# Kernel optimization log

Hardware: AMD Instinct MI355X
Metric: run time of the kernel (lower is better)

## Reference

```python
import jax, jax.numpy as jnp
import numpy as np

N = 100000      # nodes
E = 3200000     # edges (avg degree 32)
IN = 256        # in_channels
HID = 32        # hidden (hard-coded in module)
OUT = 40        # out_channels / classes
BN_EPS = 1e-5


def gcn_conv(x, W, b, src, dst, n):
    # PyG GCNConv: h = x @ W; add self-loops; symmetric norm D^-1/2 A D^-1/2; aggregate; + bias
    h = x @ W                                   # [n, d_out]
    loop = jnp.arange(n)
    s = jnp.concatenate([src, loop])            # [E+n]
    d = jnp.concatenate([dst, loop])
    deg = jax.ops.segment_sum(jnp.ones_like(d, dtype=h.dtype), d, num_segments=n)
    dinv = jnp.where(deg > 0, jax.lax.rsqrt(deg), 0.0)
    norm = dinv[s] * dinv[d]                    # [E+n]
    msg = h[s] * norm[:, None]                  # gather + scale
    return jax.ops.segment_sum(msg, d, num_segments=n) + b


def setup_inputs() -> dict:
    key = jax.random.key(0)
    k = jax.random.split(key, 4)
    x = jax.random.normal(k[0], (N, IN), dtype=jnp.float32)
    edge_index = jax.random.randint(k[1], (2, E), 0, N, dtype=jnp.int64)
    W1 = jax.random.normal(k[2], (IN, HID), dtype=jnp.float32) / np.float32(np.sqrt(IN))
    b1 = jnp.zeros((HID,), jnp.float32)
    W2 = jax.random.normal(k[3], (HID, OUT), dtype=jnp.float32) / np.float32(np.sqrt(HID))
    b2 = jnp.zeros((OUT,), jnp.float32)
    return {"x": x, "edge_index": edge_index, "W1": W1, "b1": b1, "W2": W2, "b2": b2}


def reference(x, edge_index, W1, b1, W2, b2):
    src, dst = edge_index[0], edge_index[1]
    h = jax.nn.elu(gcn_conv(x, W1, b1, src, dst, N))
    # BatchNorm1d created fresh each forward: batch stats, gamma=1, beta=0 (biased var)
    mean = jnp.mean(h, axis=0)
    var = jnp.mean((h - mean) ** 2, axis=0)
    h = (h - mean) * jax.lax.rsqrt(var + BN_EPS)
    h = jax.nn.relu(h)
    # Dropout(p=0.2): identity in eval / deterministic reference
    out = gcn_conv(h, W2, b2, src, dst, N)
    return jax.nn.log_softmax(out, axis=-1)
```

## Files before the change

kernel.cpp:

```cpp
#include <hip/hip_runtime.h>
#include <math.h>

typedef unsigned int uint;
typedef unsigned short ushort;
typedef float v2f __attribute__((ext_vector_type(2)));

__device__ __forceinline__ v2f fp8lo_to_f32(uint u) {
    return __builtin_amdgcn_cvt_pk_f32_fp8((int)u, false);
}
__device__ __forceinline__ v2f fp8hi_to_f32(uint u) {
    return __builtin_amdgcn_cvt_pk_f32_fp8((int)u, true);
}
__device__ __forceinline__ ushort f32x2_to_fp8(float a, float b) {
    return (ushort)(__builtin_amdgcn_cvt_pk_fp8_f32(a, b, 0, false) & 0xffff);
}

#define UNPACK8(r, f)                                                  \
    {                                                                  \
        v2f p0_ = fp8lo_to_f32((r).x), p1_ = fp8hi_to_f32((r).x);      \
        v2f p2_ = fp8lo_to_f32((r).y), p3_ = fp8hi_to_f32((r).y);      \
        f[0] += p0_.x; f[1] += p0_.y; f[2] += p1_.x; f[3] += p1_.y;    \
        f[4] += p2_.x; f[5] += p2_.y; f[6] += p3_.x; f[7] += p3_.y;    \
    }

#define NBU 49
#define NSEG 4
#define CELL 17408
#define SUBCAP 1280
#define CSRCAP 4608

__global__ __launch_bounds__(256) void k_bin(
    const int* __restrict__ src, const int* __restrict__ dst,
    int* __restrict__ cur, uint* __restrict__ ebuf, int E) {
    __shared__ int hist[NBU], base_[NBU], off[NBU];
    int tid = threadIdx.x;
    if (tid < NBU) { hist[tid] = 0; off[tid] = 0; }
    __syncthreads();
    int e0 = blockIdx.x * 4096 + tid;
    int s_[16], d_[16];
#pragma unroll
    for (int j = 0; j < 16; ++j) {
        int e = e0 + j * 256;
        if (e < E) {
            s_[j] = src[e]; d_[j] = dst[e];
            atomicAdd(&hist[d_[j] >> 11], 1);
        } else d_[j] = -1;
    }
    __syncthreads();
    int seg = blockIdx.x & 3;
    if (tid < NBU && hist[tid])
        base_[tid] = atomicAdd(&cur[tid * NSEG + seg], hist[tid]);
    __syncthreads();
#pragma unroll
    for (int j = 0; j < 16; ++j) {
        if (d_[j] >= 0) {
            int b = d_[j] >> 11;
            int p = base_[b] + atomicAdd(&off[b], 1);
            if (p < CELL)
                ebuf[(size_t)(b * NSEG + seg) * CELL + p] =
                    ((uint)(d_[j] & 2047) << 17) | (uint)s_[j];
        }
    }
}

__global__ __launch_bounds__(256) void k_bin2(
    const int* __restrict__ cur, const uint* __restrict__ ebuf,
    uint* __restrict__ subcell, int* __restrict__ slotlen) {
    __shared__ int curs[16], sbase[16];
    int tid = threadIdx.x;
    int b = blockIdx.x >> 2, seg = blockIdx.x & 3;
    if (tid < 16) {
        int sb = ((b * 16 + tid) * NSEG + seg) * SUBCAP;
        sbase[tid] = sb;
        curs[tid] = sb;
    }
    __syncthreads();
    int len = cur[b * NSEG + seg]; if (len > CELL) len = CELL;
    const uint* ep = ebuf + (size_t)(b * NSEG + seg) * CELL;
    int i = tid;
    for (; i + 768 < len; i += 1024) {
        uint v0 = ep[i], v1 = ep[i + 256], v2 = ep[i + 512], v3 = ep[i + 768];
        int u0 = (v0 >> 24) & 15, u1 = (v1 >> 24) & 15;
        int u2 = (v2 >> 24) & 15, u3 = (v3 >> 24) & 15;
        int p0 = atomicAdd(&curs[u0], 1);
        if (p0 - sbase[u0] < SUBCAP) subcell[p0] = v0;
        int p1 = atomicAdd(&curs[u1], 1);
        if (p1 - sbase[u1] < SUBCAP) subcell[p1] = v1;
        int p2 = atomicAdd(&curs[u2], 1);
        if (p2 - sbase[u2] < SUBCAP) subcell[p2] = v2;
        int p3 = atomicAdd(&curs[u3], 1);
        if (p3 - sbase[u3] < SUBCAP) subcell[p3] = v3;
    }
    for (; i < len; i += 256) {
        uint v = ep[i];
        int u = (v >> 24) & 15;
        int p = atomicAdd(&curs[u], 1);
        if (p - sbase[u] < SUBCAP) subcell[p] = v;
    }
    __syncthreads();
    if (tid < 16) {
        int c = curs[tid] - sbase[tid];
        slotlen[(b * 16 + tid) * NSEG + seg] = c < SUBCAP ? c : SUBCAP;
    }
}

__global__ __launch_bounds__(256) void k_sort3(
    const int* __restrict__ slotlen, const uint* __restrict__ subcell,
    uint* __restrict__ csr, int* __restrict__ rowstart, int* __restrict__ deg,
    float* __restrict__ dinv, int n) {
    __shared__ int hist[128];
    __shared__ int wtot;
    int tid = threadIdx.x;
    int bs = blockIdx.x;
    if (tid < 128) hist[tid] = 0;
    __syncthreads();
    int lens[NSEG];
    const uint* sp = subcell + (size_t)bs * NSEG * SUBCAP;
    for (int s = 0; s < NSEG; ++s) {
        int len = slotlen[bs * NSEG + s];
        lens[s] = len;
        const uint* ep = sp + s * SUBCAP;
        int i = tid;
        for (; i + 768 < len; i += 1024) {
            uint v0 = ep[i], v1 = ep[i + 256], v2 = ep[i + 512], v3 = ep[i + 768];
            atomicAdd(&hist[(v0 >> 17) & 127], 1);
            atomicAdd(&hist[(v1 >> 17) & 127], 1);
            atomicAdd(&hist[(v2 >> 17) & 127], 1);
            atomicAdd(&hist[(v3 >> 17) & 127], 1);
        }
        for (; i < len; i += 256) atomicAdd(&hist[(ep[i] >> 17) & 127], 1);
    }
    __syncthreads();
    int c = (tid < 128) ? hist[tid] : 0;
    int lane = tid & 63, w = tid >> 6;
    int incl = c;
#pragma unroll
    for (int o = 1; o < 64; o <<= 1) {
        int t = __shfl_up(incl, o, 64);
        if (lane >= o) incl += t;
    }
    if (w == 0 && lane == 63) wtot = incl;
    __syncthreads();
    int excl = incl - c + ((w == 1) ? wtot : 0);
    int csrBase = bs * CSRCAP;
    int node = bs * 128 + tid;
    if (tid < 128 && node < n) {
        deg[node] = c;
        dinv[node] = rsqrtf((float)c + 1.0f);
        rowstart[node] = csrBase + excl;
    }
    __syncthreads();
    if (tid < 128) hist[tid] = excl;
    __syncthreads();
    for (int s = 0; s < NSEG; ++s) {
        const uint* ep = sp + s * SUBCAP;
        int len = lens[s];
        int i = tid;
        for (; i + 768 < len; i += 1024) {
            uint v0 = ep[i], v1 = ep[i + 256], v2 = ep[i + 512], v3 = ep[i + 768];
            int p0 = atomicAdd(&hist[(v0 >> 17) & 127], 1);
            csr[csrBase + p0] = v0 & 0x1FFFFu;
            int p1 = atomicAdd(&hist[(v1 >> 17) & 127], 1);
            csr[csrBase + p1] = v1 & 0x1FFFFu;
            int p2 = atomicAdd(&hist[(v2 >> 17) & 127], 1);
            csr[csrBase + p2] = v2 & 0x1FFFFu;
            int p3 = atomicAdd(&hist[(v3 >> 17) & 127], 1);
            csr[csrBase + p3] = v3 & 0x1FFFFu;
        }
        for (; i < len; i += 256) {
            uint v = ep[i];
            int p = atomicAdd(&hist[(v >> 17) & 127], 1);
            csr[csrBase + p] = v & 0x1FFFFu;
        }
    }
}


__global__ __launch_bounds__(256) void k_gemm1(
    const float* __restrict__ x, const float* __restrict__ W,
    const float* __restrict__ dinv, ushort* __restrict__ h8, int n) {
    __shared__ ushort xl[64 * 256];
    int tid = threadIdx.x;
    int node0 = blockIdx.x * 64;

#pragma unroll 4
    for (int i = 0; i < 16; ++i) {
        int fidx = i * 1024 + tid * 4;
        int row = fidx >> 8, k = fidx & 255;
        uint bx = 0, by = 0;
        if (node0 + row < n) {
            float4 xv = *(const float4*)(x + (size_t)(node0 + row) * 256 + k);
            uint r0 = (__float_as_uint(xv.x) + 0x8000u) >> 16;
            uint r1 = (__float_as_uint(xv.y) + 0x8000u) >> 16;
            uint r2 = (__float_as_uint(xv.z) + 0x8000u) >> 16;
            uint r3 = (__float_as_uint(xv.w) + 0x8000u) >> 16;
            bx = r0 | (r1 << 16); by = r2 | (r3 << 16);
        }
        int g = k >> 3;
        int byteoff = row * 512 + (((g ^ (row & 31)) << 4) | ((k & 7) << 1));
        *(uint2*)((char*)xl + byteoff) = make_uint2(bx, by);
    }
    __syncthreads();

    int lane = tid & 63;
    int wv = __builtin_amdgcn_readfirstlane(tid >> 6);
    const char* xrow = (const char*)xl + lane * 512;
    int rx = lane & 31;
    const float* Wp = W + wv * 8;
    float acc[8];
#pragma unroll
    for (int c = 0; c < 8; ++c) acc[c] = 0.f;
#pragma unroll 2
    for (int g = 0; g < 32; ++g) {
        uint4 q = *(const uint4*)(xrow + (((g ^ rx) << 4)));
        float xe[8];
        xe[0] = __uint_as_float(q.x << 16);
        xe[1] = __uint_as_float(q.x & 0xFFFF0000u);
        xe[2] = __uint_as_float(q.y << 16);
        xe[3] = __uint_as_float(q.y & 0xFFFF0000u);
        xe[4] = __uint_as_float(q.z << 16);
        xe[5] = __uint_as_float(q.z & 0xFFFF0000u);
        xe[6] = __uint_as_float(q.w << 16);
        xe[7] = __uint_as_float(q.w & 0xFFFF0000u);
        const float* w0 = Wp + (size_t)(g * 8) * 32;
#pragma unroll
        for (int e = 0; e < 8; ++e) {
#pragma unroll
            for (int c = 0; c < 8; ++c) acc[c] += xe[e] * w0[e * 32 + c];
        }
    }
    int node = node0 + lane;
    if (node < n) {
        float di = dinv[node];
        ushort u0 = f32x2_to_fp8(acc[0] * di, acc[1] * di);
        ushort u1 = f32x2_to_fp8(acc[2] * di, acc[3] * di);
        ushort u2 = f32x2_to_fp8(acc[4] * di, acc[5] * di);
        ushort u3 = f32x2_to_fp8(acc[6] * di, acc[7] * di);
        uint2 p;
        p.x = (uint)u0 | ((uint)u1 << 16);
        p.y = (uint)u2 | ((uint)u3 << 16);
        *((uint2*)(h8 + (size_t)node * 16) + wv) = p;
    }
}

__global__ __launch_bounds__(256) void k_agg1(
    const ushort* __restrict__ hs, const int* __restrict__ deg,
    const int* __restrict__ rowstart, const uint* __restrict__ csr,
    const float* __restrict__ dinv, const float* __restrict__ b1,
    ushort* __restrict__ y, float* __restrict__ partials, int n) {
    int tid = threadIdx.x;
    int l4 = tid & 3;
    int g  = tid >> 2;
    int d  = blockIdx.x * 64 + g;
    float sa[8], qa[8];
#pragma unroll
    for (int j = 0; j < 8; ++j) { sa[j] = 0.f; qa[j] = 0.f; }
    if (d < n) {
        float a[8], c[8];
#pragma unroll
        for (int j = 0; j < 8; ++j) { a[j] = 0.f; c[j] = 0.f; }
        uint2 sr = *((const uint2*)(hs + (size_t)d * 16) + l4);
        UNPACK8(sr, a);
        const uint* row = csr + rowstart[d];
        int end = deg[d];
        int k = 0;
        for (; k + 4 <= end; k += 4) {
            uint s0 = row[k], s1 = row[k+1], s2 = row[k+2], s3 = row[k+3];
            uint2 r0 = *((const uint2*)(hs + (size_t)s0 * 16) + l4);
            uint2 r1 = *((const uint2*)(hs + (size_t)s1 * 16) + l4);
            uint2 r2 = *((const uint2*)(hs + (size_t)s2 * 16) + l4);
            uint2 r3 = *((const uint2*)(hs + (size_t)s3 * 16) + l4);
            UNPACK8(r0, a); UNPACK8(r1, c);
            UNPACK8(r2, a); UNPACK8(r3, c);
        }
        for (; k < end; ++k) {
            uint2 r = *((const uint2*)(hs + (size_t)row[k] * 16) + l4);
            UNPACK8(r, a);
        }
        float di = dinv[d];
        float4 bA = *(const float4*)(b1 + l4 * 8);
        float4 bB = *(const float4*)(b1 + l4 * 8 + 4);
        float bv[8] = {bA.x, bA.y, bA.z, bA.w, bB.x, bB.y, bB.z, bB.w};
        float vv[8];
#pragma unroll
        for (int j = 0; j < 8; ++j) {
            float v = di * (a[j] + c[j]) + bv[j];
            v = v > 0.f ? v : expm1f(v);
            vv[j] = v; sa[j] = v; qa[j] = v * v;
        }
        ushort u0 = f32x2_to_fp8(vv[0], vv[1]);
        ushort u1 = f32x2_to_fp8(vv[2], vv[3]);
        ushort u2 = f32x2_to_fp8(vv[4], vv[5]);
        ushort u3 = f32x2_to_fp8(vv[6], vv[7]);
        uint2 pw;
        pw.x = (uint)u0 | ((uint)u1 << 16);
        pw.y = (uint)u2 | ((uint)u3 << 16);
        *((uint2*)(y + (size_t)d * 16) + l4) = pw;
    }
#pragma unroll
    for (int m = 4; m <= 32; m <<= 1) {
#pragma unroll
        for (int j = 0; j < 8; ++j) {
            sa[j] += __shfl_xor(sa[j], m, 64);
            qa[j] += __shfl_xor(qa[j], m, 64);
        }
    }
    __shared__ float wred[4][4][16];
    int lane = tid & 63, wv = tid >> 6;
    if (lane < 4) {
#pragma unroll
        for (int j = 0; j < 8; ++j) {
            wred[wv][lane][j]     = sa[j];
            wred[wv][lane][8 + j] = qa[j];
        }
    }
    __syncthreads();
    if (tid < 64) {
        int l4g = tid >> 4, slot = tid & 15;
        partials[(size_t)blockIdx.x * 64 + tid] =
            wred[0][l4g][slot] + wred[1][l4g][slot] +
            wred[2][l4g][slot] + wred[3][l4g][slot];
    }
}

__global__ __launch_bounds__(1024) void k_red(
    const float* __restrict__ partials, float* __restrict__ stats, int nblk) {
    __shared__ float red[1024];
    int t = threadIdx.x;
    int j = t & 63, w = t >> 6;
    float a = 0.f;
    for (int i = w; i < nblk; i += 16) a += partials[(size_t)i * 64 + j];
    red[t] = a;
    __syncthreads();
    if (t < 64) {
        float v = 0.f;
#pragma unroll
        for (int kk = 0; kk < 16; ++kk) v += red[kk * 64 + t];
        int l4g = t >> 4, slot = t & 15, c = l4g * 8 + (slot & 7);
        stats[(slot < 8) ? c : (32 + c)] = v;
    }
}

__global__ void k_bn2(const ushort* __restrict__ y, const float* __restrict__ stats,
                      const float* __restrict__ dinv, ushort* __restrict__ h2s, int n) {
    int t = blockIdx.x * blockDim.x + threadIdx.x;
    if (t >= n * 16) return;
    int i = t >> 4, c2 = (t & 15) * 2;
    float invn = 1.0f / (float)n;
    float m0 = stats[c2] * invn,    m1 = stats[c2+1] * invn;
    float v0 = stats[32+c2] * invn - m0*m0;
    float v1 = stats[33+c2] * invn - m1*m1;
    float s0 = rsqrtf(v0 + 1e-5f), s1 = rsqrtf(v1 + 1e-5f);
    float di = dinv[i];
    v2f u = fp8lo_to_f32(y[t]);
    float a = (u.x - m0) * s0; a = a > 0.f ? a : 0.f; a *= di;
    float b = (u.y - m1) * s1; b = b > 0.f ? b : 0.f; b *= di;
    h2s[t] = f32x2_to_fp8(a, b);
}

__global__ __launch_bounds__(256) void k_agg2(
    const ushort* __restrict__ h2s, const int* __restrict__ deg,
    const int* __restrict__ rowstart, const uint* __restrict__ csr,
    const float* __restrict__ dinv, const float* __restrict__ W2,
    const float* __restrict__ b2, float* __restrict__ out, int n) {
    __shared__ float w2s[1280];
    __shared__ float b2s[40];
    __shared__ float tb[64][33];
    int tid = threadIdx.x;
    for (int t = tid; t < 1280; t += 256) w2s[t] = W2[t];
    if (tid < 40) b2s[tid] = b2[tid];
    int l4 = tid & 3, g = tid >> 2;
    int d = blockIdx.x * 64 + g;
    if (d < n) {
        float a[8], c[8];
#pragma unroll
        for (int j = 0; j < 8; ++j) { a[j] = 0.f; c[j] = 0.f; }
        uint2 sr = *((const uint2*)(h2s + (size_t)d * 16) + l4);
        UNPACK8(sr, a);
        const uint* row = csr + rowstart[d];
        int end = deg[d];
        int k = 0;
        for (; k + 4 <= end; k += 4) {
            uint s0 = row[k], s1 = row[k+1], s2 = row[k+2], s3 = row[k+3];
            uint2 r0 = *((const uint2*)(h2s + (size_t)s0 * 16) + l4);
            uint2 r1 = *((const uint2*)(h2s + (size_t)s1 * 16) + l4);
            uint2 r2 = *((const uint2*)(h2s + (size_t)s2 * 16) + l4);
            uint2 r3 = *((const uint2*)(h2s + (size_t)s3 * 16) + l4);
            UNPACK8(r0, a); UNPACK8(r1, c);
            UNPACK8(r2, a); UNPACK8(r3, c);
        }
        for (; k < end; ++k) {
            uint2 r = *((const uint2*)(h2s + (size_t)row[k] * 16) + l4);
            UNPACK8(r, a);
        }
        float di = dinv[d];
#pragma unroll
        for (int j = 0; j < 8; ++j) tb[g][l4 * 8 + j] = di * (a[j] + c[j]);
    }
    __syncthreads();
    float o[10];
    const float* bp = b2s + l4 * 10;
#pragma unroll
    for (int m = 0; m < 10; ++m) o[m] = bp[m];
#pragma unroll
    for (int cc = 0; cc < 32; ++cc) {
        float tc = tb[g][cc];
        const float* wr = w2s + cc * 40 + l4 * 10;
#pragma unroll
        for (int m = 0; m < 10; ++m) o[m] += tc * wr[m];
    }
    float mx = o[0];
#pragma unroll
    for (int m = 1; m < 10; ++m) mx = fmaxf(mx, o[m]);
    mx = fmaxf(mx, __shfl_xor(mx, 1, 64));
    mx = fmaxf(mx, __shfl_xor(mx, 2, 64));
    float s = 0.f;
#pragma unroll
    for (int m = 0; m < 10; ++m) s += __expf(o[m] - mx);
    s += __shfl_xor(s, 1, 64);
    s += __shfl_xor(s, 2, 64);
    float lse = mx + __logf(s);
    if (d < n) {
        float* r = out + (size_t)d * 40 + l4 * 10;
#pragma unroll
        for (int m = 0; m < 10; m += 2) {
            float2 wv;
            wv.x = o[m] - lse; wv.y = o[m+1] - lse;
            *(float2*)(r + m) = wv;
        }
    }
}


extern "C" void kernel_launch(void* const* d_in, const int* in_sizes, int n_in,
                              void* d_out, int out_size, void* d_ws, size_t ws_size,
                              hipStream_t stream) {
    const float* x  = (const float*)d_in[0];
    const int*   ei = (const int*)d_in[1];
    const float* W1 = (const float*)d_in[2];
    const float* b1 = (const float*)d_in[3];
    const float* W2 = (const float*)d_in[4];
    const float* b2 = (const float*)d_in[5];

    int n = in_sizes[0] / 256;
    int E = in_sizes[1] / 2;
    const int* src = ei;
    const int* dst = ei + E;

    char*   base    = (char*)d_ws;
    ushort* hs8     = (ushort*)base;
    ushort* y       = (ushort*)(base + (size_t)n * 32);
    ushort* h2s     = (ushort*)(base + (size_t)n * 64);
    float*  dinv    = (float*) (base + (size_t)n * 96);
    int*    deg     = (int*)   (base + (size_t)n * 100);
    int*    rowstart= (int*)   (base + (size_t)n * 104);
    float*  stats   = (float*) (base + (size_t)n * 108);
    int*    cur     = (int*)   (base + (size_t)n * 108 + 256);
    int*    slotlen = (int*)   (base + (size_t)n * 108 + 1280);
    float*  partials= (float*) (base + (size_t)n * 108 + 13824);
    uint*   ebuf    = (uint*)  (base + (size_t)n * 108 + 538112);
    size_t  ebufB   = (size_t)NBU * NSEG * CELL * 4;
    uint*   subcell = (uint*)  ((char*)ebuf + ebufB);
    size_t  subB    = (size_t)NBU * 16 * NSEG * SUBCAP * 4;
    uint*   csr     = (uint*)  ((char*)subcell + subB);
    float*  out     = (float*)d_out;

    const int B = 256;
    int nb64 = (n + 63) / 64;

    hipMemsetAsync(cur, 0, NBU * NSEG * sizeof(int), stream);

    k_bin  <<<(E + 4095) / 4096, B, 0, stream>>>(src, dst, cur, ebuf, E);
    k_bin2 <<<NBU * NSEG, B, 0, stream>>>(cur, ebuf, subcell, slotlen);
    k_sort3<<<NBU * 16, B, 0, stream>>>(slotlen, subcell, csr, rowstart, deg,
                                        dinv, n);

    k_gemm1<<<(n + 63) / 64, B, 0, stream>>>(x, W1, dinv, hs8, n);
    k_agg1 <<<nb64, B, 0, stream>>>(hs8, deg, rowstart, csr, dinv, b1, y,
                                    partials, n);
    k_red  <<<1, 1024, 0, stream>>>(partials, stats, nb64);

    k_bn2<<<(n * 16 + B - 1) / B, B, 0, stream>>>(y, stats, dinv, h2s, n);

    k_agg2<<<nb64, B, 0, stream>>>(h2s, deg, rowstart, csr, dinv, W2, b2, out, n);
}
```

Before: 396.9 us.

## Compute first-layer GEMM with bf16 MFMA instead of scalar FMA loops

```diff
diff --git a/kernel.cpp b/kernel.cpp
--- a/kernel.cpp
+++ b/kernel.cpp
@@ -4,6 +4,8 @@
 typedef unsigned int uint;
 typedef unsigned short ushort;
 typedef float v2f __attribute__((ext_vector_type(2)));
+typedef __attribute__((ext_vector_type(8))) short bf16x8;
+typedef __attribute__((ext_vector_type(4))) float f32x4;
 
 __device__ __forceinline__ v2f fp8lo_to_f32(uint u) {
     return __builtin_amdgcn_cvt_pk_f32_fp8((int)u, false);
@@ -180,6 +182,7 @@
     const float* __restrict__ x, const float* __restrict__ W,
     const float* __restrict__ dinv, ushort* __restrict__ h8, int n) {
     __shared__ ushort xl[64 * 256];
+    __shared__ ushort wt[32 * 256];
     int tid = threadIdx.x;
     int node0 = blockIdx.x * 64;
 
@@ -197,49 +200,60 @@
             bx = r0 | (r1 << 16); by = r2 | (r3 << 16);
         }
         int g = k >> 3;
-        int byteoff = row * 512 + (((g ^ (row & 31)) << 4) | ((k & 7) << 1));
+        int byteoff = row * 512 + ((((g ^ row) & 31) << 4) | ((k & 7) << 1));
         *(uint2*)((char*)xl + byteoff) = make_uint2(bx, by);
     }
+#pragma unroll
+    for (int i = 0; i < 32; ++i) {
+        int idx = i * 256 + tid;
+        int k = idx >> 5, c = idx & 31;
+        uint b = (__float_as_uint(W[idx]) + 0x8000u) >> 16;
+        int byteoff = c * 512 + ((((k >> 3) ^ c) & 31) << 4) + ((k & 7) << 1);
+        *(ushort*)((char*)wt + byteoff) = (ushort)b;
+    }
     __syncthreads();
 
     int lane = tid & 63;
-    int wv = __builtin_amdgcn_readfirstlane(tid >> 6);
-    const char* xrow = (const char*)xl + lane * 512;
-    int rx = lane & 31;
-    const float* Wp = W + wv * 8;
-    float acc[8];
-#pragma unroll
-    for (int c = 0; c < 8; ++c) acc[c] = 0.f;
-#pragma unroll 2
-    for (int g = 0; g < 32; ++g) {
-        uint4 q = *(const uint4*)(xrow + (((g ^ rx) << 4)));
-        float xe[8];
-        xe[0] = __uint_as_float(q.x << 16);
-        xe[1] = __uint_as_float(q.x & 0xFFFF0000u);
-        xe[2] = __uint_as_float(q.y << 16);
-        xe[3] = __uint_as_float(q.y & 0xFFFF0000u);
-        xe[4] = __uint_as_float(q.z << 16);
-        xe[5] = __uint_as_float(q.z & 0xFFFF0000u);
-        xe[6] = __uint_as_float(q.w << 16);
-        xe[7] = __uint_as_float(q.w & 0xFFFF0000u);
-        const float* w0 = Wp + (size_t)(g * 8) * 32;
-#pragma unroll
-        for (int e = 0; e < 8; ++e) {
-#pragma unroll
-            for (int c = 0; c < 8; ++c) acc[c] += xe[e] * w0[e * 32 + c];
-        }
-    }
-    int node = node0 + lane;
+    int w = tid >> 6;
+    int l15 = lane & 15, h = lane >> 4;
+    int ra = 16 * w + l15;
+    const char* arow = (const char*)xl + ra * 512;
+    const char* b0row = (const char*)wt + l15 * 512;
+    const char* b1row = (const char*)wt + (16 + l15) * 512;
+    int ram = ra & 31, c0m = l15, c1m = 16 + l15;
+    f32x4 acc0 = {0.f, 0.f, 0.f, 0.f}, acc1 = {0.f, 0.f, 0.f, 0.f};
+#pragma unroll
+    for (int kk = 0; kk < 8; ++kk) {
+        int g = 4 * kk + h;
+        bf16x8 av = *(const bf16x8*)(arow + (((g ^ ram) & 31) << 4));
+        bf16x8 b0 = *(const bf16x8*)(b0row + (((g ^ c0m) & 31) << 4));
+        bf16x8 b1 = *(const bf16x8*)(b1row + (((g ^ c1m) & 31) << 4));
+        acc0 = __builtin_amdgcn_mfma_f32_16x16x32_bf16(av, b0, acc0, 0, 0, 0);
+        acc1 = __builtin_amdgcn_mfma_f32_16x16x32_bf16(av, b1, acc1, 0, 0, 0);
+    }
+    __syncthreads();
+    float* ol = (float*)xl;
+    int rb = 16 * w + h * 4;
+#pragma unroll
+    for (int r = 0; r < 4; ++r) {
+        ol[(rb + r) * 33 + l15]      = acc0[r];
+        ol[(rb + r) * 33 + l15 + 16] = acc1[r];
+    }
+    __syncthreads();
+
+    int g2 = tid >> 2, oct = tid & 3;
+    int node = node0 + g2;
     if (node < n) {
         float di = dinv[node];
-        ushort u0 = f32x2_to_fp8(acc[0] * di, acc[1] * di);
-        ushort u1 = f32x2_to_fp8(acc[2] * di, acc[3] * di);
-        ushort u2 = f32x2_to_fp8(acc[4] * di, acc[5] * di);
-        ushort u3 = f32x2_to_fp8(acc[6] * di, acc[7] * di);
+        const float* orow = ol + g2 * 33 + oct * 8;
+        ushort u0 = f32x2_to_fp8(orow[0] * di, orow[1] * di);
+        ushort u1 = f32x2_to_fp8(orow[2] * di, orow[3] * di);
+        ushort u2 = f32x2_to_fp8(orow[4] * di, orow[5] * di);
+        ushort u3 = f32x2_to_fp8(orow[6] * di, orow[7] * di);
         uint2 p;
         p.x = (uint)u0 | ((uint)u1 << 16);
         p.y = (uint)u2 | ((uint)u3 << 16);
-        *((uint2*)(h8 + (size_t)node * 16) + wv) = p;
+        *((uint2*)(h8 + (size_t)node * 16) + oct) = p;
     }
 }
 
```

Result: faster. 364.9 us (-8.1%).
